# Kernel optimization log

Measured on AMD Instinct MI355X. Metric: run time of the kernel, lower is better.

Reference implementation:

```python
import jax, jax.numpy as jnp
import numpy as np

DIM = 128
NUM_HEADS = 8


def setup_inputs() -> dict:
    key = jax.random.key(0)
    ks = jax.random.split(key, 5)
    B, L, C = 4, 16384, DIM
    x = jax.random.normal(ks[0], (B, L, C), dtype=jnp.float32)
    # Linear params (stored as (in, out) so y = x @ W + b)
    w_qkv = jax.random.normal(ks[1], (C, 3 * C), dtype=jnp.float32) * (C ** -0.5)
    b_qkv = jax.random.normal(ks[2], (3 * C,), dtype=jnp.float32) * 0.02
    w_proj = jax.random.normal(ks[3], (C, C), dtype=jnp.float32) * (C ** -0.5)
    b_proj = jax.random.normal(ks[4], (C,), dtype=jnp.float32) * 0.02
    return {"x": x, "w_qkv": w_qkv, "b_qkv": b_qkv, "w_proj": w_proj, "b_proj": b_proj}


def reference(x, w_qkv, b_qkv, w_proj, b_proj):
    B, L, C = x.shape
    H = NUM_HEADS
    hd = C // H
    scale = C ** -0.5  # note: torch code scales by dim**-0.5, not head_dim**-0.5

    qkv = x @ w_qkv + b_qkv                      # (B, L, 3C)
    q, k, v = jnp.split(qkv, 3, axis=-1)         # each (B, L, C)

    def to_heads(t):
        return t.reshape(B, L, H, hd).transpose(0, 2, 1, 3)  # (B, H, L, hd)

    q, k, v = to_heads(q), to_heads(k), to_heads(v)

    # Per-token outer product over head_dim: (B, H, L, hd, hd)
    attn = (q * scale)[..., :, None] * k[..., None, :]
    attn = jax.nn.softmax(attn, axis=-1)

    # attn @ v per token: (B, H, L, hd)
    out = jnp.einsum("bhlij,bhlj->bhli", attn, v)
    out = out.transpose(0, 2, 1, 3).reshape(B, L, C)  # (B, L, C)
    return out @ w_proj + b_proj
```

## Files before the change

kernel.cpp:

```cpp
#include <hip/hip_runtime.h>


typedef __attribute__((ext_vector_type(8))) short bf16x8;
typedef __attribute__((ext_vector_type(4))) float f32x4;

#define TILE_M 32
#define QKV_STRIDE 392
#define O_STRIDE 136

__device__ __forceinline__ unsigned short f2bf(float f) {
    unsigned int u = __builtin_bit_cast(unsigned int, f);
    u += 0x7fffu + ((u >> 16) & 1u);
    return (unsigned short)(u >> 16);
}
__device__ __forceinline__ float bf2f(unsigned short h) {
    unsigned int u = ((unsigned int)h) << 16;
    return __builtin_bit_cast(float, u);
}

__global__ void prep_weights(const float* __restrict__ wqkv,
                             const float* __restrict__ wproj,
                             unsigned short* __restrict__ wqkvT,
                             unsigned short* __restrict__ wprojT) {
    int idx = blockIdx.x * 256 + threadIdx.x;
    if (idx < 384 * 128) {
        int n = idx >> 7, k = idx & 127;
        wqkvT[idx] = f2bf(wqkv[k * 384 + n]);
    }
    if (idx < 128 * 128) {
        int n = idx >> 7, k = idx & 127;
        wprojT[idx] = f2bf(wproj[k * 128 + n]);
    }
}

__global__ __launch_bounds__(256, 5) void fused_channel_attn(
    const float* __restrict__ x,
    const unsigned short* __restrict__ wqkvT,
    const float* __restrict__ bqkv,
    const unsigned short* __restrict__ wprojT,
    const float* __restrict__ bproj,
    float* __restrict__ out)
{
    __shared__ __align__(16) unsigned short us[TILE_M * QKV_STRIDE];

    const int tid  = threadIdx.x;
    const int lane = tid & 63;
    const int wave = tid >> 6;
    const int col  = lane & 15;
    const int quad = lane >> 4;
    const long base_tok = (long)blockIdx.x * TILE_M;

    const int m  = wave & 1;
    const int nb = (wave >> 1) * 12;

    const float* xrow = x + (base_tok + m * 16 + col) * 128;
    bf16x8 afr[4];
#pragma unroll
    for (int ks = 0; ks < 4; ++ks) {
        const float4* p = (const float4*)(xrow + ks * 32 + quad * 8);
        float4 f0 = p[0], f1 = p[1];
        bf16x8 a;
        a[0] = f2bf(f0.x); a[1] = f2bf(f0.y); a[2] = f2bf(f0.z); a[3] = f2bf(f0.w);
        a[4] = f2bf(f1.x); a[5] = f2bf(f1.y); a[6] = f2bf(f1.z); a[7] = f2bf(f1.w);
        afr[ks] = a;
    }

    f32x4 acc[12];
#pragma unroll
    for (int j = 0; j < 12; ++j) {
        float b = bqkv[(nb + j) * 16 + col];
        acc[j] = (f32x4){b, b, b, b};
    }
#pragma unroll
    for (int ks = 0; ks < 4; ++ks) {
#pragma unroll
        for (int j = 0; j < 12; ++j) {
            bf16x8 bfrag = *(const bf16x8*)&wqkvT[((nb + j) * 16 + col) * 128 + ks * 32 + quad * 8];
            acc[j] = __builtin_amdgcn_mfma_f32_16x16x32_bf16(afr[ks], bfrag, acc[j], 0, 0, 0);
        }
    }

#pragma unroll
    for (int j = 0; j < 12; ++j)
#pragma unroll
        for (int r = 0; r < 4; ++r)
            us[(m * 16 + quad * 4 + r) * QKV_STRIDE + (nb + j) * 16 + col] = f2bf(acc[j][r]);
    __syncthreads();

    const int t = tid & 31;
    const int h = tid >> 5;
    const unsigned short* qrow = &us[t * QKV_STRIDE + h * 16];

    bf16x8 qr  = *(const bf16x8*)(qrow);
    bf16x8 qr2 = *(const bf16x8*)(qrow + 8);
    bf16x8 kr  = *(const bf16x8*)(qrow + 128);
    bf16x8 kr2 = *(const bf16x8*)(qrow + 136);
    bf16x8 vr  = *(const bf16x8*)(qrow + 256);
    bf16x8 vr2 = *(const bf16x8*)(qrow + 264);
    __syncthreads();

    const float sl2e = 0.08838834764831845f * 1.44269504088896340f;
    float kf[16], vf[16];
#pragma unroll
    for (int j = 0; j < 8; ++j) {
        kf[j]     = bf2f((unsigned short)kr[j]);
        kf[j + 8] = bf2f((unsigned short)kr2[j]);
        vf[j]     = bf2f((unsigned short)vr[j]);
        vf[j + 8] = bf2f((unsigned short)vr2[j]);
    }
    bf16x8 o0, o1;
#pragma unroll
    for (int i = 0; i < 16; ++i) {
        float qs = bf2f((unsigned short)(i < 8 ? qr[i & 7] : qr2[i & 7])) * sl2e;
        float den = 0.f, num = 0.f;
#pragma unroll
        for (int j = 0; j < 16; ++j) {
            float e = __builtin_amdgcn_exp2f(qs * kf[j]);
            den += e;
            num = fmaf(e, vf[j], num);
        }
        unsigned short ob = f2bf(num * __builtin_amdgcn_rcpf(den));
        if (i < 8) o0[i] = (short)ob; else o1[i & 7] = (short)ob;
    }
    *(bf16x8*)&us[t * O_STRIDE + h * 16]     = o0;
    *(bf16x8*)&us[t * O_STRIDE + h * 16 + 8] = o1;
    __syncthreads();

    const int nb2 = (wave >> 1) * 4;
    bf16x8 af[4];
#pragma unroll
    for (int ks = 0; ks < 4; ++ks)
        af[ks] = *(const bf16x8*)&us[(m * 16 + col) * O_STRIDE + ks * 32 + quad * 8];

    f32x4 acc2[4];
#pragma unroll
    for (int n = 0; n < 4; ++n) {
        float b = bproj[(nb2 + n) * 16 + col];
        acc2[n] = (f32x4){b, b, b, b};
    }
#pragma unroll
    for (int ks = 0; ks < 4; ++ks) {
#pragma unroll
        for (int n = 0; n < 4; ++n) {
            bf16x8 bfrag = *(const bf16x8*)&wprojT[((nb2 + n) * 16 + col) * 128 + ks * 32 + quad * 8];
            acc2[n] = __builtin_amdgcn_mfma_f32_16x16x32_bf16(af[ks], bfrag, acc2[n], 0, 0, 0);
        }
    }
#pragma unroll
    for (int n = 0; n < 4; ++n)
#pragma unroll
        for (int r = 0; r < 4; ++r) {
            long tt = base_tok + m * 16 + quad * 4 + r;
            out[tt * 128 + (nb2 + n) * 16 + col] = acc2[n][r];
        }
}

extern "C" void kernel_launch(void* const* d_in, const int* in_sizes, int n_in,
                              void* d_out, int out_size, void* d_ws, size_t ws_size,
                              hipStream_t stream) {
    const float* x     = (const float*)d_in[0];
    const float* wqkv  = (const float*)d_in[1];
    const float* bqkv  = (const float*)d_in[2];
    const float* wproj = (const float*)d_in[3];
    const float* bproj = (const float*)d_in[4];
    float* out = (float*)d_out;

    unsigned short* wqkvT  = (unsigned short*)d_ws;
    unsigned short* wprojT = wqkvT + 384 * 128;

    prep_weights<<<192, 256, 0, stream>>>(wqkv, wproj, wqkvT, wprojT);

    const int tokens = in_sizes[0] / 128;
    fused_channel_attn<<<tokens / TILE_M, 256, 0, stream>>>(
        x, wqkvT, bqkv, wprojT, bproj, out);
}
```

Baseline: 157.3 us.

## Give each wave both token rows to halve weight-fragment loads in both GEMMs

Each wave now covers both 16-token M tiles and a narrower slice of output columns (6 instead of 12 for QKV, 2 instead of 4 for proj). Every weight fragment loaded from global memory is therefore reused for two MFMAs, which halves per-wave weight traffic. All x loads are issued up front before conversion so they can be in flight together. The cost is more registers (x staging, two A fragments, doubled accumulators), so launch bounds drop from 5 to 4 waves per SIMD, lowering occupancy.

```diff
diff --git a/kernel.cpp b/kernel.cpp
--- a/kernel.cpp
+++ b/kernel.cpp
@@ -33,7 +33,7 @@
     }
 }
 
-__global__ __launch_bounds__(256, 5) void fused_channel_attn(
+__global__ __launch_bounds__(256, 4) void fused_channel_attn(
     const float* __restrict__ x,
     const unsigned short* __restrict__ wqkvT,
     const float* __restrict__ bqkv,
@@ -50,41 +50,58 @@
     const int quad = lane >> 4;
     const long base_tok = (long)blockIdx.x * TILE_M;
 
-    const int m  = wave & 1;
-    const int nb = (wave >> 1) * 12;
-
-    const float* xrow = x + (base_tok + m * 16 + col) * 128;
-    bf16x8 afr[4];
+    const int nb = wave * 6;
+
+    float4 xf[2][4][2];
+#pragma unroll
+    for (int m = 0; m < 2; ++m) {
+        const float* xrow = x + (base_tok + m * 16 + col) * 128;
+#pragma unroll
+        for (int ks = 0; ks < 4; ++ks) {
+            const float4* p = (const float4*)(xrow + ks * 32 + quad * 8);
+            xf[m][ks][0] = p[0];
+            xf[m][ks][1] = p[1];
+        }
+    }
+    bf16x8 afr[2][4];
+#pragma unroll
+    for (int m = 0; m < 2; ++m)
+#pragma unroll
+        for (int ks = 0; ks < 4; ++ks) {
+            float4 f0 = xf[m][ks][0], f1 = xf[m][ks][1];
+            bf16x8 a;
+            a[0] = f2bf(f0.x); a[1] = f2bf(f0.y); a[2] = f2bf(f0.z); a[3] = f2bf(f0.w);
+            a[4] = f2bf(f1.x); a[5] = f2bf(f1.y); a[6] = f2bf(f1.z); a[7] = f2bf(f1.w);
+            afr[m][ks] = a;
+        }
+
+    f32x4 acc[2][6];
+#pragma unroll
+    for (int j = 0; j < 6; ++j) {
+        float b = bqkv[(nb + j) * 16 + col];
+        acc[0][j] = (f32x4){b, b, b, b};
+        acc[1][j] = (f32x4){b, b, b, b};
+    }
 #pragma unroll
     for (int ks = 0; ks < 4; ++ks) {
-        const float4* p = (const float4*)(xrow + ks * 32 + quad * 8);
-        float4 f0 = p[0], f1 = p[1];
-        bf16x8 a;
-        a[0] = f2bf(f0.x); a[1] = f2bf(f0.y); a[2] = f2bf(f0.z); a[3] = f2bf(f0.w);
-        a[4] = f2bf(f1.x); a[5] = f2bf(f1.y); a[6] = f2bf(f1.z); a[7] = f2bf(f1.w);
-        afr[ks] = a;
-    }
-
-    f32x4 acc[12];
-#pragma unroll
-    for (int j = 0; j < 12; ++j) {
-        float b = bqkv[(nb + j) * 16 + col];
-        acc[j] = (f32x4){b, b, b, b};
-    }
-#pragma unroll
-    for (int ks = 0; ks < 4; ++ks) {
-#pragma unroll
-        for (int j = 0; j < 12; ++j) {
-            bf16x8 bfrag = *(const bf16x8*)&wqkvT[((nb + j) * 16 + col) * 128 + ks * 32 + quad * 8];
-            acc[j] = __builtin_amdgcn_mfma_f32_16x16x32_bf16(afr[ks], bfrag, acc[j], 0, 0, 0);
-        }
-    }
-
-#pragma unroll
-    for (int j = 0; j < 12; ++j)
-#pragma unroll
-        for (int r = 0; r < 4; ++r)
-            us[(m * 16 + quad * 4 + r) * QKV_STRIDE + (nb + j) * 16 + col] = f2bf(acc[j][r]);
+        bf16x8 bfr[6];
+#pragma unroll
+        for (int j = 0; j < 6; ++j)
+            bfr[j] = *(const bf16x8*)&wqkvT[((nb + j) * 16 + col) * 128 + ks * 32 + quad * 8];
+#pragma unroll
+        for (int j = 0; j < 6; ++j) {
+            acc[0][j] = __builtin_amdgcn_mfma_f32_16x16x32_bf16(afr[0][ks], bfr[j], acc[0][j], 0, 0, 0);
+            acc[1][j] = __builtin_amdgcn_mfma_f32_16x16x32_bf16(afr[1][ks], bfr[j], acc[1][j], 0, 0, 0);
+        }
+    }
+
+#pragma unroll
+    for (int m = 0; m < 2; ++m)
+#pragma unroll
+        for (int j = 0; j < 6; ++j)
+#pragma unroll
+            for (int r = 0; r < 4; ++r)
+                us[(m * 16 + quad * 4 + r) * QKV_STRIDE + (nb + j) * 16 + col] = f2bf(acc[m][j][r]);
     __syncthreads();
 
     const int t = tid & 31;
@@ -126,33 +143,42 @@
     *(bf16x8*)&us[t * O_STRIDE + h * 16 + 8] = o1;
     __syncthreads();
 
-    const int nb2 = (wave >> 1) * 4;
-    bf16x8 af[4];
-#pragma unroll
-    for (int ks = 0; ks < 4; ++ks)
-        af[ks] = *(const bf16x8*)&us[(m * 16 + col) * O_STRIDE + ks * 32 + quad * 8];
-
-    f32x4 acc2[4];
-#pragma unroll
-    for (int n = 0; n < 4; ++n) {
+    const int nb2 = wave * 2;
+    bf16x8 af2[2][4];
+#pragma unroll
+    for (int m = 0; m < 2; ++m)
+#pragma unroll
+        for (int ks = 0; ks < 4; ++ks)
+            af2[m][ks] = *(const bf16x8*)&us[(m * 16 + col) * O_STRIDE + ks * 32 + quad * 8];
+
+    f32x4 acc2[2][2];
+#pragma unroll
+    for (int n = 0; n < 2; ++n) {
         float b = bproj[(nb2 + n) * 16 + col];
-        acc2[n] = (f32x4){b, b, b, b};
+        acc2[0][n] = (f32x4){b, b, b, b};
+        acc2[1][n] = (f32x4){b, b, b, b};
     }
 #pragma unroll
     for (int ks = 0; ks < 4; ++ks) {
-#pragma unroll
-        for (int n = 0; n < 4; ++n) {
-            bf16x8 bfrag = *(const bf16x8*)&wprojT[((nb2 + n) * 16 + col) * 128 + ks * 32 + quad * 8];
-            acc2[n] = __builtin_amdgcn_mfma_f32_16x16x32_bf16(af[ks], bfrag, acc2[n], 0, 0, 0);
-        }
-    }
-#pragma unroll
-    for (int n = 0; n < 4; ++n)
-#pragma unroll
-        for (int r = 0; r < 4; ++r) {
-            long tt = base_tok + m * 16 + quad * 4 + r;
-            out[tt * 128 + (nb2 + n) * 16 + col] = acc2[n][r];
-        }
+        bf16x8 bb[2];
+#pragma unroll
+        for (int n = 0; n < 2; ++n)
+            bb[n] = *(const bf16x8*)&wprojT[((nb2 + n) * 16 + col) * 128 + ks * 32 + quad * 8];
+#pragma unroll
+        for (int n = 0; n < 2; ++n) {
+            acc2[0][n] = __builtin_amdgcn_mfma_f32_16x16x32_bf16(af2[0][ks], bb[n], acc2[0][n], 0, 0, 0);
+            acc2[1][n] = __builtin_amdgcn_mfma_f32_16x16x32_bf16(af2[1][ks], bb[n], acc2[1][n], 0, 0, 0);
+        }
+    }
+#pragma unroll
+    for (int m = 0; m < 2; ++m)
+#pragma unroll
+        for (int n = 0; n < 2; ++n)
+#pragma unroll
+            for (int r = 0; r < 4; ++r) {
+                long tt = base_tok + m * 16 + quad * 4 + r;
+                out[tt * 128 + (nb2 + n) * 16 + col] = acc2[m][n][r];
+            }
 }
 
 extern "C" void kernel_launch(void* const* d_in, const int* in_sizes, int n_in,
```

Measured after the change: 136.8 us. 1.15x faster.
